# Kernel tuning notes

Measured on AMD Instinct MI355X. Metric: run time of the kernel, lower is better.

Reference implementation:

```python
import jax, jax.numpy as jnp
import numpy as np

B, C, H, W = 16, 1024, 48, 48
MID = 512
EPS = 1e-5


def _conv1x1(x, Wt, b):
    # x: [B,C,H,W], Wt: [O,C], b: [O] -> [B,O,H,W]
    return jnp.einsum('bchw,oc->bohw', x, Wt) + b[None, :, None, None]


def _bn_relu(y, gamma, beta, mean, var):
    inv = gamma / jnp.sqrt(var + EPS)
    return jax.nn.relu(y * inv[None, :, None, None] + (beta - mean * inv)[None, :, None, None])


def setup_inputs() -> dict:
    key = jax.random.key(0)
    ks = jax.random.split(key, 17)
    d = {
        'x': jax.random.normal(ks[0], (B, C, H, W), jnp.float32),
        'Wf': jax.random.normal(ks[1], (MID, C), jnp.float32) * (2.0 / C) ** 0.5,
        'bf': jax.random.normal(ks[2], (MID,), jnp.float32) * 0.1,
        'gf': jax.random.uniform(ks[3], (MID,), jnp.float32, 0.5, 1.5),
        'betaf': jax.random.normal(ks[4], (MID,), jnp.float32) * 0.1,
        'mf': jax.random.normal(ks[5], (MID,), jnp.float32) * 0.1,
        'vf': jax.random.uniform(ks[6], (MID,), jnp.float32, 0.5, 1.5),
        'Wg': jax.random.normal(ks[7], (MID, C), jnp.float32) * (2.0 / C) ** 0.5,
        'bg': jax.random.normal(ks[8], (MID,), jnp.float32) * 0.1,
        'gg': jax.random.uniform(ks[9], (MID,), jnp.float32, 0.5, 1.5),
        'betag': jax.random.normal(ks[10], (MID,), jnp.float32) * 0.1,
        'mg': jax.random.normal(ks[11], (MID,), jnp.float32) * 0.1,
        'vg': jax.random.uniform(ks[12], (MID,), jnp.float32, 0.5, 1.5),
        'Wh': jax.random.normal(ks[13], (MID, C), jnp.float32) * (2.0 / C) ** 0.5,
        'bh': jax.random.normal(ks[14], (MID,), jnp.float32) * 0.1,
        'Wv': jax.random.normal(ks[15], (C, MID), jnp.float32) * (2.0 / MID) ** 0.5,
        'bv': jax.random.normal(ks[16], (C,), jnp.float32) * 0.1,
    }
    return d


def reference(x, Wf, bf, gf, betaf, mf, vf, Wg, bg, gg, betag, mg, vg, Wh, bh, Wv, bv):
    b, c, h, w = x.shape
    n = h * w
    mid = Wf.shape[0]
    f_x = _bn_relu(_conv1x1(x, Wf, bf), gf, betaf, mf, vf).reshape(b, mid, n)  # [B,mid,N]
    g_x = _bn_relu(_conv1x1(x, Wg, bg), gg, betag, mg, vg).reshape(b, mid, n)  # [B,mid,N]
    h_x = _conv1x1(x, Wh, bh).reshape(b, mid, n)                               # [B,mid,N]
    # z = f_x^T @ g_x : [B,N,N]
    z = jnp.einsum('bmi,bmj->bij', f_x, g_x)
    attn = jax.nn.softmax(z * (mid ** -0.5), axis=-1)
    # attn @ h_x^T : [B,N,mid]
    out = jnp.einsum('bij,bmj->bim', attn, h_x)
    out = out.transpose(0, 2, 1).reshape(b, mid, h, w)
    out = _conv1x1(out, Wv, bv) + x  # residual
    return out
```

## Files before the change

### kernel.cpp

```cpp
#include <hip/hip_runtime.h>
#include <hip/hip_bf16.h>

#define BN_  16
#define CH   1024
#define MIDC 512
#define NPIX 2304

typedef __bf16 bf16x8 __attribute__((ext_vector_type(8)));
typedef __bf16 bf16x4 __attribute__((ext_vector_type(4)));
typedef float  f32x4  __attribute__((ext_vector_type(4)));

typedef __attribute__((address_space(1))) void void_g;
typedef __attribute__((address_space(3))) void void_l;

__device__ __forceinline__ void gll16(const void* g, void* l) {
  __builtin_amdgcn_global_load_lds((const void_g*)g, (void_l*)l, 16, 0, 0);
}

template<int EPI>
__global__ __launch_bounds__(256)
void gemm_bt(const __hip_bfloat16* __restrict__ Ag, int lda, long sA,
             const __hip_bfloat16* __restrict__ Bg, int ldb, long sB,
             void* __restrict__ Cg, int ldc, long sC,
             int K,
             const float* __restrict__ e0, const float* __restrict__ e1,
             const float* __restrict__ resid, long sR, float fscale)
{
  __shared__ __align__(16) __hip_bfloat16 lA[128 * 64];
  __shared__ __align__(16) __hip_bfloat16 lB[128 * 64];
  const int tid  = threadIdx.x;
  const int lane = tid & 63;
  const int wave = tid >> 6;

  const int gx = gridDim.x, gy = gridDim.y;
  const int nwg = gx * gy * gridDim.z;
  const int L  = blockIdx.x + gx * (blockIdx.y + gy * blockIdx.z);
  const int wg = (L & 7) * (nwg >> 3) + (L >> 3);
  const int pb = gx * gy;
  const int bz = wg / pb;
  const int rem = wg - bz * pb;
  const int m0 = (rem % gx) * 128;
  const int n0 = (rem / gx) * 128;

  const int srow = tid >> 3;
  const int schk = (tid & 7) ^ (srow & 7);
  const __hip_bfloat16* Ab = Ag + (long)bz * sA + (long)(m0 + srow) * lda + schk * 8;
  const __hip_bfloat16* Bb = Bg + (long)bz * sB + (long)(n0 + srow) * ldb + schk * 8;
  __hip_bfloat16* lAw = lA + wave * 512;
  __hip_bfloat16* lBw = lB + wave * 512;

  const int wr = wave >> 1, wc = wave & 1;
  const int fr = lane & 15;
  const int fc = lane >> 4;

  f32x4 acc[4][4] = {};

  for (int k0 = 0; k0 < K; k0 += 64) {
#pragma unroll
    for (int c = 0; c < 4; ++c) {
      gll16(Ab + k0 + (long)c * 32 * lda, lAw + c * 2048);
      gll16(Bb + k0 + (long)c * 32 * ldb, lBw + c * 2048);
    }
    __syncthreads();
#pragma unroll
    for (int kk = 0; kk < 2; ++kk) {
      bf16x8 af[4], bfv[4];
#pragma unroll
      for (int i = 0; i < 4; ++i) {
        const int ra = wr * 64 + i * 16 + fr;
        af[i]  = *(const bf16x8*)(lA + ra * 64 + (((kk * 4 + fc) ^ (fr & 7)) * 8));
        const int rb = wc * 64 + i * 16 + fr;
        bfv[i] = *(const bf16x8*)(lB + rb * 64 + (((kk * 4 + fc) ^ (fr & 7)) * 8));
      }
#pragma unroll
      for (int mi = 0; mi < 4; ++mi)
#pragma unroll
        for (int ni = 0; ni < 4; ++ni)
          acc[mi][ni] = __builtin_amdgcn_mfma_f32_16x16x32_bf16(af[mi], bfv[ni], acc[mi][ni], 0, 0, 0);
    }
    __syncthreads();
  }

  const int rbase = m0 + wr * 64 + (lane >> 4) * 4;
  const int cbase = n0 + wc * 64 + fr;
  if constexpr (EPI == 4) {
    float* Cb = (float*)Cg + (long)bz * sC;
    const float* Rb = resid + (long)bz * sR;
#pragma unroll
    for (int mi = 0; mi < 4; ++mi) {
#pragma unroll
      for (int r = 0; r < 4; ++r) {
        const int row = rbase + mi * 16 + r;
        const float bias = e0[row];
#pragma unroll
        for (int ni = 0; ni < 4; ++ni) {
          const long idx = (long)row * ldc + cbase + ni * 16;
          Cb[idx] = acc[mi][ni][r] + bias + Rb[idx];
        }
      }
    }
  } else {
    __hip_bfloat16* Cb = (__hip_bfloat16*)Cg + (long)bz * sC;
#pragma unroll
    for (int mi = 0; mi < 4; ++mi) {
#pragma unroll
      for (int r = 0; r < 4; ++r) {
        const int row = rbase + mi * 16 + r;
#pragma unroll
        for (int ni = 0; ni < 4; ++ni) {
          const int col = cbase + ni * 16;
          float v = acc[mi][ni][r];
          if constexpr (EPI == 1) { v = fmaxf(v * e0[col] + e1[col], 0.f); }
          if constexpr (EPI == 2) { v += e0[row]; }
          if constexpr (EPI == 3) { v *= fscale; }
          Cb[(long)row * ldc + col] = __float2bfloat16(v);
        }
      }
    }
  }
}

__global__ __launch_bounds__(256)
void softmax_rows(__hip_bfloat16* __restrict__ z)
{
  const long row = blockIdx.x;
  __hip_bfloat16* p = z + row * NPIX;
  const int t = threadIdx.x;
  const int lane = t & 63, wave = t >> 6;

  float v[9];
  bf16x8 pk = *(const bf16x8*)(p + t * 8);
#pragma unroll
  for (int i = 0; i < 8; ++i) v[i] = (float)pk[i];
  v[8] = __bfloat162float(p[2048 + t]);

  float mx = v[0];
#pragma unroll
  for (int i = 1; i < 9; ++i) mx = fmaxf(mx, v[i]);
#pragma unroll
  for (int o = 32; o > 0; o >>= 1) mx = fmaxf(mx, __shfl_xor(mx, o));
  __shared__ float redm[4], reds[4];
  if (lane == 0) redm[wave] = mx;
  __syncthreads();
  mx = fmaxf(fmaxf(redm[0], redm[1]), fmaxf(redm[2], redm[3]));

  float s = 0.f;
#pragma unroll
  for (int i = 0; i < 9; ++i) { v[i] = __expf(v[i] - mx); s += v[i]; }
#pragma unroll
  for (int o = 32; o > 0; o >>= 1) s += __shfl_xor(s, o);
  if (lane == 0) reds[wave] = s;
  __syncthreads();
  s = reds[0] + reds[1] + reds[2] + reds[3];
  const float inv = 1.f / s;

  bf16x8 ok;
#pragma unroll
  for (int i = 0; i < 8; ++i) ok[i] = (__bf16)(v[i] * inv);
  *(bf16x8*)(p + t * 8) = ok;
  p[2048 + t] = __float2bfloat16(v[8] * inv);
}

__global__ __launch_bounds__(256)
void transpose_cvt(const float* __restrict__ x, __hip_bfloat16* __restrict__ xt)
{
  __shared__ float tile[64 * 65];
  const int n0 = blockIdx.x * 64, c0 = blockIdx.y * 64;
  const long bo = (long)blockIdx.z * CH * NPIX;
  const int t = threadIdx.x;
#pragma unroll
  for (int i = 0; i < 16; ++i) {
    const int idx = i * 256 + t;
    const int cl = idx >> 6, nl = idx & 63;
    tile[cl * 65 + nl] = x[bo + (long)(c0 + cl) * NPIX + n0 + nl];
  }
  __syncthreads();
#pragma unroll
  for (int i = 0; i < 16; ++i) {
    const int idx = i * 256 + t;
    const int nl = idx >> 6, cl = idx & 63;
    xt[bo + (long)(n0 + nl) * CH + c0 + cl] = __float2bfloat16(tile[cl * 65 + nl]);
  }
}

__global__ __launch_bounds__(256)
void cvt4(const float* __restrict__ a, const float* __restrict__ b,
          const float* __restrict__ c, const float* __restrict__ d,
          __hip_bfloat16* oa, __hip_bfloat16* ob,
          __hip_bfloat16* oc, __hip_bfloat16* od)
{
  const int i = (blockIdx.x * 256 + threadIdx.x) * 4;
  const float* s; __hip_bfloat16* o;
  switch (blockIdx.y) {
    case 0:  s = a; o = oa; break;
    case 1:  s = b; o = ob; break;
    case 2:  s = c; o = oc; break;
    default: s = d; o = od; break;
  }
  const float4 v = *(const float4*)(s + i);
  bf16x4 w;
  w[0] = (__bf16)v.x; w[1] = (__bf16)v.y; w[2] = (__bf16)v.z; w[3] = (__bf16)v.w;
  *(bf16x4*)(o + i) = w;
}

__global__ void prep_scales(const float* bf_, const float* gf, const float* bef,
                            const float* mf, const float* vf,
                            const float* bg_, const float* gg, const float* beg,
                            const float* mg, const float* vg,
                            float* sc, float* sh)
{
  const int r = blockIdx.x * 256 + threadIdx.x;
  if (r >= 1024) return;
  int j; const float *b, *g, *be, *m, *vv;
  if (r < 512) { b = bf_; g = gf; be = bef; m = mf; vv = vf; j = r; }
  else         { b = bg_; g = gg; be = beg; m = mg; vv = vg; j = r - 512; }
  const float inv = g[j] / sqrtf(vv[j] + 1e-5f);
  sc[r] = inv;
  sh[r] = (b[j] - m[j]) * inv + be[j];
}

extern "C" void kernel_launch(void* const* d_in, const int* in_sizes, int n_in,
                              void* d_out, int out_size, void* d_ws, size_t ws_size,
                              hipStream_t stream)
{
  const float* x     = (const float*)d_in[0];
  const float* Wf    = (const float*)d_in[1];
  const float* bf_   = (const float*)d_in[2];
  const float* gf    = (const float*)d_in[3];
  const float* betaf = (const float*)d_in[4];
  const float* mf    = (const float*)d_in[5];
  const float* vf    = (const float*)d_in[6];
  const float* Wg    = (const float*)d_in[7];
  const float* bg_   = (const float*)d_in[8];
  const float* gg    = (const float*)d_in[9];
  const float* betag = (const float*)d_in[10];
  const float* mg    = (const float*)d_in[11];
  const float* vg    = (const float*)d_in[12];
  const float* Wh    = (const float*)d_in[13];
  const float* bh    = (const float*)d_in[14];
  const float* Wv    = (const float*)d_in[15];
  const float* bv    = (const float*)d_in[16];
  float* out = (float*)d_out;
  (void)in_sizes; (void)n_in; (void)out_size; (void)ws_size;

  char* ws = (char*)d_ws;
  size_t off = 0;
  auto take = [&](size_t bytes) -> char* {
    char* p = ws + off;
    off += (bytes + 255) & ~(size_t)255;
    return p;
  };
  __hip_bfloat16* xt   = (__hip_bfloat16*)take((size_t)BN_ * NPIX * CH * 2);
  __hip_bfloat16* fgT  = (__hip_bfloat16*)take((size_t)BN_ * NPIX * 1024 * 2);
  __hip_bfloat16* hbuf = (__hip_bfloat16*)take((size_t)BN_ * MIDC * NPIX * 2);
  __hip_bfloat16* om   = (__hip_bfloat16*)take((size_t)BN_ * NPIX * MIDC * 2);
  __hip_bfloat16* zat  = (__hip_bfloat16*)take((size_t)BN_ * NPIX * NPIX * 2);
  __hip_bfloat16* Wfgb = (__hip_bfloat16*)take((size_t)1024 * CH * 2);
  __hip_bfloat16* Whb  = (__hip_bfloat16*)take((size_t)MIDC * CH * 2);
  __hip_bfloat16* Wvb  = (__hip_bfloat16*)take((size_t)CH * MIDC * 2);
  float* scfg = (float*)take(1024 * 4);
  float* shfg = (float*)take(1024 * 4);

  prep_scales<<<dim3(4), dim3(256), 0, stream>>>(bf_, gf, betaf, mf, vf,
                                                 bg_, gg, betag, mg, vg, scfg, shfg);
  cvt4<<<dim3(512, 4), dim3(256), 0, stream>>>(Wf, Wg, Wh, Wv,
                                               Wfgb, Wfgb + 512 * 1024, Whb, Wvb);
  transpose_cvt<<<dim3(36, 16, BN_), dim3(256), 0, stream>>>(x, xt);

  gemm_bt<1><<<dim3(18, 8, BN_), dim3(256), 0, stream>>>(
      xt, CH, (long)NPIX * CH, Wfgb, CH, 0L,
      fgT, 1024, (long)NPIX * 1024, CH,
      scfg, shfg, nullptr, 0L, 0.f);

  gemm_bt<2><<<dim3(4, 18, BN_), dim3(256), 0, stream>>>(
      Whb, CH, 0L, xt, CH, (long)NPIX * CH,
      hbuf, NPIX, (long)MIDC * NPIX, CH,
      bh, nullptr, nullptr, 0L, 0.f);

  gemm_bt<3><<<dim3(18, 18, BN_), dim3(256), 0, stream>>>(
      fgT, 1024, (long)NPIX * 1024, fgT + 512, 1024, (long)NPIX * 1024,
      zat, NPIX, (long)NPIX * NPIX, MIDC,
      nullptr, nullptr, nullptr, 0L, 0.044194173824159216f);

  softmax_rows<<<dim3(BN_ * NPIX), dim3(256), 0, stream>>>(zat);

  gemm_bt<0><<<dim3(18, 4, BN_), dim3(256), 0, stream>>>(
      zat, NPIX, (long)NPIX * NPIX, hbuf, NPIX, (long)MIDC * NPIX,
      om, MIDC, (long)NPIX * MIDC, NPIX,
      nullptr, nullptr, nullptr, 0L, 0.f);

  gemm_bt<4><<<dim3(8, 18, BN_), dim3(256), 0, stream>>>(
      Wvb, MIDC, 0L, om, MIDC, (long)NPIX * MIDC,
      out, NPIX, (long)CH * NPIX, MIDC,
      bv, nullptr, x, (long)CH * NPIX, 0.f);
}
```

Before: 604.9 us.

## Replace 128x128 GEMM with double-buffered 256x256 tile, 8-wave kernel

The GEMM moves from 128x128 tiles with 4 waves and single-buffered LDS to 256x256 tiles with 8 waves and a double-buffered 128KB LDS. Global-to-LDS loads for the next K-step are interleaved with the MFMA phases, and s_setprio raises priority during the MFMA bursts. The aim is more data reuse per tile and overlap of memory loads with compute, replacing the full syncthreads stalls. In exchange, each workgroup holds more accumulator registers and LDS, so occupancy drops to one block per CU, and the small GEMMs launch fewer workgroups.

```diff
diff --git a/kernel.cpp b/kernel.cpp
--- a/kernel.cpp
+++ b/kernel.cpp
@@ -18,19 +18,18 @@
 }
 
 template<int EPI>
-__global__ __launch_bounds__(256)
-void gemm_bt(const __hip_bfloat16* __restrict__ Ag, int lda, long sA,
+__global__ __launch_bounds__(512)
+void gemm256(const __hip_bfloat16* __restrict__ Ag, int lda, long sA,
              const __hip_bfloat16* __restrict__ Bg, int ldb, long sB,
              void* __restrict__ Cg, int ldc, long sC,
              int K,
              const float* __restrict__ e0, const float* __restrict__ e1,
              const float* __restrict__ resid, long sR, float fscale)
 {
-  __shared__ __align__(16) __hip_bfloat16 lA[128 * 64];
-  __shared__ __align__(16) __hip_bfloat16 lB[128 * 64];
-  const int tid  = threadIdx.x;
-  const int lane = tid & 63;
-  const int wave = tid >> 6;
+  __shared__ __align__(16) __hip_bfloat16 lds[65536];
+  const int tid = threadIdx.x;
+  const int l   = tid & 63;
+  const int w   = tid >> 6;
 
   const int gx = gridDim.x, gy = gridDim.y;
   const int nwg = gx * gy * gridDim.z;
@@ -39,62 +38,95 @@
   const int pb = gx * gy;
   const int bz = wg / pb;
   const int rem = wg - bz * pb;
-  const int m0 = (rem % gx) * 128;
-  const int n0 = (rem / gx) * 128;
-
-  const int srow = tid >> 3;
-  const int schk = (tid & 7) ^ (srow & 7);
+  const int m0 = (rem % gx) * 256;
+  const int n0 = (rem / gx) * 256;
+
+  const int srow = w * 8 + (l >> 3);
+  const int schk = (l & 7) ^ (l >> 3);
   const __hip_bfloat16* Ab = Ag + (long)bz * sA + (long)(m0 + srow) * lda + schk * 8;
   const __hip_bfloat16* Bb = Bg + (long)bz * sB + (long)(n0 + srow) * ldb + schk * 8;
-  __hip_bfloat16* lAw = lA + wave * 512;
-  __hip_bfloat16* lBw = lB + wave * 512;
-
-  const int wr = wave >> 1, wc = wave & 1;
-  const int fr = lane & 15;
-  const int fc = lane >> 4;
-
-  f32x4 acc[4][4] = {};
-
-  for (int k0 = 0; k0 < K; k0 += 64) {
-#pragma unroll
-    for (int c = 0; c < 4; ++c) {
-      gll16(Ab + k0 + (long)c * 32 * lda, lAw + c * 2048);
-      gll16(Bb + k0 + (long)c * 32 * ldb, lBw + c * 2048);
+  const int stg = w * 512;
+
+  auto stageA = [&](int buf, int half, long kofs) {
+    __hip_bfloat16* d = lds + buf * 16384 + half * 8192 + stg;
+    gll16(Ab + kofs + (long)(half * 128) * lda,      d);
+    gll16(Ab + kofs + (long)(half * 128 + 64) * lda, d + 4096);
+  };
+  auto stageB = [&](int buf, int half, long kofs) {
+    __hip_bfloat16* d = lds + 32768 + buf * 16384 + half * 8192 + stg;
+    gll16(Bb + kofs + (long)(half * 128) * ldb,      d);
+    gll16(Bb + kofs + (long)(half * 128 + 64) * ldb, d + 4096);
+  };
+
+  const int wr = w >> 2, wc = w & 3;
+  const int fr = l & 15;
+  const int fc = l >> 4;
+  const int slot0 = ((fc)     ^ (fr & 7)) * 8;
+  const int slot1 = ((4 + fc) ^ (fr & 7)) * 8;
+
+  f32x4 acc[8][4] = {};
+
+  stageA(0, 0, 0); stageA(0, 1, 0); stageB(0, 0, 0); stageB(0, 1, 0);
+  asm volatile("s_waitcnt vmcnt(0)" ::: "memory");
+  __builtin_amdgcn_s_barrier();
+
+  const int NT = K >> 6;
+  for (int t = 0; t < NT; ++t) {
+    const __hip_bfloat16* lAc = lds + (t & 1) * 16384;
+    const __hip_bfloat16* lBc = lds + 32768 + (t & 1) * 16384;
+    const int  nb   = (t & 1) ^ 1;
+    const long knxt = (long)(t + 1) * 64;
+    const bool more = (t + 1 < NT);
+#pragma unroll
+    for (int p = 0; p < 4; ++p) {
+      const int mh = p >> 1, nh = p & 1;
+      bf16x8 avA[4][2], avB[2][2];
+#pragma unroll
+      for (int i = 0; i < 4; ++i) {
+        const int row = wr * 128 + (mh * 4 + i) * 16 + fr;
+        avA[i][0] = *(const bf16x8*)(lAc + row * 64 + slot0);
+        avA[i][1] = *(const bf16x8*)(lAc + row * 64 + slot1);
+      }
+#pragma unroll
+      for (int j = 0; j < 2; ++j) {
+        const int row = wc * 64 + (nh * 2 + j) * 16 + fr;
+        avB[j][0] = *(const bf16x8*)(lBc + row * 64 + slot0);
+        avB[j][1] = *(const bf16x8*)(lBc + row * 64 + slot1);
+      }
+      if (more) {
+        if (p < 2) stageA(nb, p, knxt); else stageB(nb, p - 2, knxt);
+      }
+      __builtin_amdgcn_s_barrier();
+      __builtin_amdgcn_s_setprio(1);
+#pragma unroll
+      for (int i = 0; i < 4; ++i)
+#pragma unroll
+        for (int j = 0; j < 2; ++j) {
+          acc[mh * 4 + i][nh * 2 + j] = __builtin_amdgcn_mfma_f32_16x16x32_bf16(
+              avA[i][0], avB[j][0], acc[mh * 4 + i][nh * 2 + j], 0, 0, 0);
+          acc[mh * 4 + i][nh * 2 + j] = __builtin_amdgcn_mfma_f32_16x16x32_bf16(
+              avA[i][1], avB[j][1], acc[mh * 4 + i][nh * 2 + j], 0, 0, 0);
+        }
+      __builtin_amdgcn_s_setprio(0);
+      if (p == 3) asm volatile("s_waitcnt vmcnt(0)" ::: "memory");
+      __builtin_amdgcn_s_barrier();
     }
-    __syncthreads();
-#pragma unroll
-    for (int kk = 0; kk < 2; ++kk) {
-      bf16x8 af[4], bfv[4];
-#pragma unroll
-      for (int i = 0; i < 4; ++i) {
-        const int ra = wr * 64 + i * 16 + fr;
-        af[i]  = *(const bf16x8*)(lA + ra * 64 + (((kk * 4 + fc) ^ (fr & 7)) * 8));
-        const int rb = wc * 64 + i * 16 + fr;
-        bfv[i] = *(const bf16x8*)(lB + rb * 64 + (((kk * 4 + fc) ^ (fr & 7)) * 8));
-      }
-#pragma unroll
-      for (int mi = 0; mi < 4; ++mi)
-#pragma unroll
-        for (int ni = 0; ni < 4; ++ni)
-          acc[mi][ni] = __builtin_amdgcn_mfma_f32_16x16x32_bf16(af[mi], bfv[ni], acc[mi][ni], 0, 0, 0);
-    }
-    __syncthreads();
-  }
-
-  const int rbase = m0 + wr * 64 + (lane >> 4) * 4;
-  const int cbase = n0 + wc * 64 + fr;
+  }
+
+  const int rb0 = m0 + wr * 128 + (l >> 4) * 4;
+  const int cb0 = n0 + wc * 64 + fr;
   if constexpr (EPI == 4) {
     float* Cb = (float*)Cg + (long)bz * sC;
     const float* Rb = resid + (long)bz * sR;
 #pragma unroll
-    for (int mi = 0; mi < 4; ++mi) {
+    for (int mi = 0; mi < 8; ++mi) {
 #pragma unroll
       for (int r = 0; r < 4; ++r) {
-        const int row = rbase + mi * 16 + r;
+        const int row = rb0 + mi * 16 + r;
         const float bias = e0[row];
 #pragma unroll
         for (int ni = 0; ni < 4; ++ni) {
-          const long idx = (long)row * ldc + cbase + ni * 16;
+          const long idx = (long)row * ldc + cb0 + ni * 16;
           Cb[idx] = acc[mi][ni][r] + bias + Rb[idx];
         }
       }
@@ -102,13 +134,13 @@
   } else {
     __hip_bfloat16* Cb = (__hip_bfloat16*)Cg + (long)bz * sC;
 #pragma unroll
-    for (int mi = 0; mi < 4; ++mi) {
+    for (int mi = 0; mi < 8; ++mi) {
 #pragma unroll
       for (int r = 0; r < 4; ++r) {
-        const int row = rbase + mi * 16 + r;
+        const int row = rb0 + mi * 16 + r;
 #pragma unroll
         for (int ni = 0; ni < 4; ++ni) {
-          const int col = cbase + ni * 16;
+          const int col = cb0 + ni * 16;
           float v = acc[mi][ni][r];
           if constexpr (EPI == 1) { v = fmaxf(v * e0[col] + e1[col], 0.f); }
           if constexpr (EPI == 2) { v += e0[row]; }
@@ -198,9 +230,9 @@
     default: s = d; o = od; break;
   }
   const float4 v = *(const float4*)(s + i);
-  bf16x4 w;
-  w[0] = (__bf16)v.x; w[1] = (__bf16)v.y; w[2] = (__bf16)v.z; w[3] = (__bf16)v.w;
-  *(bf16x4*)(o + i) = w;
+  bf16x4 wv;
+  wv[0] = (__bf16)v.x; wv[1] = (__bf16)v.y; wv[2] = (__bf16)v.z; wv[3] = (__bf16)v.w;
+  *(bf16x4*)(o + i) = wv;
 }
 
 __global__ void prep_scales(const float* bf_, const float* gf, const float* bef,
@@ -267,29 +299,29 @@
                                                Wfgb, Wfgb + 512 * 1024, Whb, Wvb);
   transpose_cvt<<<dim3(36, 16, BN_), dim3(256), 0, stream>>>(x, xt);
 
-  gemm_bt<1><<<dim3(18, 8, BN_), dim3(256), 0, stream>>>(
+  gemm256<1><<<dim3(9, 4, BN_), dim3(512), 0, stream>>>(
       xt, CH, (long)NPIX * CH, Wfgb, CH, 0L,
       fgT, 1024, (long)NPIX * 1024, CH,
       scfg, shfg, nullptr, 0L, 0.f);
 
-  gemm_bt<2><<<dim3(4, 18, BN_), dim3(256), 0, stream>>>(
+  gemm256<2><<<dim3(2, 9, BN_), dim3(512), 0, stream>>>(
       Whb, CH, 0L, xt, CH, (long)NPIX * CH,
       hbuf, NPIX, (long)MIDC * NPIX, CH,
       bh, nullptr, nullptr, 0L, 0.f);
 
-  gemm_bt<3><<<dim3(18, 18, BN_), dim3(256), 0, stream>>>(
+  gemm256<3><<<dim3(9, 9, BN_), dim3(512), 0, stream>>>(
       fgT, 1024, (long)NPIX * 1024, fgT + 512, 1024, (long)NPIX * 1024,
       zat, NPIX, (long)NPIX * NPIX, MIDC,
       nullptr, nullptr, nullptr, 0L, 0.044194173824159216f);
 
   softmax_rows<<<dim3(BN_ * NPIX), dim3(256), 0, stream>>>(zat);
 
-  gemm_bt<0><<<dim3(18, 4, BN_), dim3(256), 0, stream>>>(
+  gemm256<0><<<dim3(9, 2, BN_), dim3(512), 0, stream>>>(
       zat, NPIX, (long)NPIX * NPIX, hbuf, NPIX, (long)MIDC * NPIX,
       om, MIDC, (long)NPIX * MIDC, NPIX,
       nullptr, nullptr, nullptr, 0L, 0.f);
 
-  gemm_bt<4><<<dim3(8, 18, BN_), dim3(256), 0, stream>>>(
+  gemm256<4><<<dim3(4, 9, BN_), dim3(512), 0, stream>>>(
       Wvb, MIDC, 0L, om, MIDC, (long)NPIX * MIDC,
       out, NPIX, (long)CH * NPIX, MIDC,
       bv, nullptr, x, (long)CH * NPIX, 0.f);
```

After: 681.7 us. +12.7%, slower.

## Fuse softmax exponent into QK GEMM epilogue and defer normalization to PV GEMM

Applied to the files above, without the earlier changes.

The attention score GEMM epilogue now computes exp2 of the scaled logits directly, stores the unnormalized values, and writes per-tile partial row sums. A small kernel reduces the partials to inverse row sums, which the PV GEMM epilogue applies to each output row. This removes the standalone softmax pass that read and rewrote the full NxN score matrix. It drops the max-subtraction, so it relies on the logits being small enough not to overflow in exp.

```diff
diff --git a/kernel.cpp b/kernel.cpp
--- a/kernel.cpp
+++ b/kernel.cpp
@@ -5,6 +5,7 @@
 #define CH   1024
 #define MIDC 512
 #define NPIX 2304
+#define NCHK 36
 
 typedef __bf16 bf16x8 __attribute__((ext_vector_type(8)));
 typedef __bf16 bf16x4 __attribute__((ext_vector_type(4)));
@@ -24,7 +25,8 @@
              void* __restrict__ Cg, int ldc, long sC,
              int K,
              const float* __restrict__ e0, const float* __restrict__ e1,
-             const float* __restrict__ resid, long sR, float fscale)
+             const float* __restrict__ resid, long sR, float fscale,
+             float* __restrict__ pw)
 {
   __shared__ __align__(16) __hip_bfloat16 lA[128 * 64];
   __shared__ __align__(16) __hip_bfloat16 lB[128 * 64];
@@ -99,6 +101,27 @@
         }
       }
     }
+  } else if constexpr (EPI == 6) {
+    __hip_bfloat16* Cb = (__hip_bfloat16*)Cg + (long)bz * sC;
+    float* pp = pw + ((long)bz * NCHK + (n0 >> 6) + wc) * NPIX;
+#pragma unroll
+    for (int mi = 0; mi < 4; ++mi) {
+#pragma unroll
+      for (int r = 0; r < 4; ++r) {
+        const int row = rbase + mi * 16 + r;
+        float rs = 0.f;
+#pragma unroll
+        for (int ni = 0; ni < 4; ++ni) {
+          const int col = cbase + ni * 16;
+          const float ev = exp2f(acc[mi][ni][r] * fscale);
+          rs += ev;
+          Cb[(long)row * ldc + col] = __float2bfloat16(ev);
+        }
+#pragma unroll
+        for (int o = 1; o < 16; o <<= 1) rs += __shfl_xor(rs, o);
+        if (fr == 0) pp[row] = rs;
+      }
+    }
   } else {
     __hip_bfloat16* Cb = (__hip_bfloat16*)Cg + (long)bz * sC;
 #pragma unroll
@@ -106,13 +129,15 @@
 #pragma unroll
       for (int r = 0; r < 4; ++r) {
         const int row = rbase + mi * 16 + r;
+        float rsc = 0.f;
+        if constexpr (EPI == 5) { rsc = e0[(long)bz * NPIX + row]; }
 #pragma unroll
         for (int ni = 0; ni < 4; ++ni) {
           const int col = cbase + ni * 16;
           float v = acc[mi][ni][r];
           if constexpr (EPI == 1) { v = fmaxf(v * e0[col] + e1[col], 0.f); }
           if constexpr (EPI == 2) { v += e0[row]; }
-          if constexpr (EPI == 3) { v *= fscale; }
+          if constexpr (EPI == 5) { v *= rsc; }
           Cb[(long)row * ldc + col] = __float2bfloat16(v);
         }
       }
@@ -121,44 +146,15 @@
 }
 
 __global__ __launch_bounds__(256)
-void softmax_rows(__hip_bfloat16* __restrict__ z)
-{
-  const long row = blockIdx.x;
-  __hip_bfloat16* p = z + row * NPIX;
-  const int t = threadIdx.x;
-  const int lane = t & 63, wave = t >> 6;
-
-  float v[9];
-  bf16x8 pk = *(const bf16x8*)(p + t * 8);
-#pragma unroll
-  for (int i = 0; i < 8; ++i) v[i] = (float)pk[i];
-  v[8] = __bfloat162float(p[2048 + t]);
-
-  float mx = v[0];
-#pragma unroll
-  for (int i = 1; i < 9; ++i) mx = fmaxf(mx, v[i]);
-#pragma unroll
-  for (int o = 32; o > 0; o >>= 1) mx = fmaxf(mx, __shfl_xor(mx, o));
-  __shared__ float redm[4], reds[4];
-  if (lane == 0) redm[wave] = mx;
-  __syncthreads();
-  mx = fmaxf(fmaxf(redm[0], redm[1]), fmaxf(redm[2], redm[3]));
-
+void reduce_invs(const float* __restrict__ pp, float* __restrict__ invS)
+{
+  const int row = blockIdx.x * 256 + threadIdx.x;
+  const int b   = blockIdx.y;
+  const float* p = pp + (long)b * NCHK * NPIX;
   float s = 0.f;
 #pragma unroll
-  for (int i = 0; i < 9; ++i) { v[i] = __expf(v[i] - mx); s += v[i]; }
-#pragma unroll
-  for (int o = 32; o > 0; o >>= 1) s += __shfl_xor(s, o);
-  if (lane == 0) reds[wave] = s;
-  __syncthreads();
-  s = reds[0] + reds[1] + reds[2] + reds[3];
-  const float inv = 1.f / s;
-
-  bf16x8 ok;
-#pragma unroll
-  for (int i = 0; i < 8; ++i) ok[i] = (__bf16)(v[i] * inv);
-  *(bf16x8*)(p + t * 8) = ok;
-  p[2048 + t] = __float2bfloat16(v[8] * inv);
+  for (int c = 0; c < NCHK; ++c) s += p[(long)c * NPIX + row];
+  invS[(long)b * NPIX + row] = 1.f / s;
 }
 
 __global__ __launch_bounds__(256)
@@ -198,9 +194,9 @@
     default: s = d; o = od; break;
   }
   const float4 v = *(const float4*)(s + i);
-  bf16x4 w;
-  w[0] = (__bf16)v.x; w[1] = (__bf16)v.y; w[2] = (__bf16)v.z; w[3] = (__bf16)v.w;
-  *(bf16x4*)(o + i) = w;
+  bf16x4 wv;
+  wv[0] = (__bf16)v.x; wv[1] = (__bf16)v.y; wv[2] = (__bf16)v.z; wv[3] = (__bf16)v.w;
+  *(bf16x4*)(o + i) = wv;
 }
 
 __global__ void prep_scales(const float* bf_, const float* gf, const float* bef,
@@ -260,6 +256,8 @@
   __hip_bfloat16* Wvb  = (__hip_bfloat16*)take((size_t)CH * MIDC * 2);
   float* scfg = (float*)take(1024 * 4);
   float* shfg = (float*)take(1024 * 4);
+  float* partials = (float*)take((size_t)BN_ * NCHK * NPIX * 4);
+  float* invS     = (float*)take((size_t)BN_ * NPIX * 4);
 
   prep_scales<<<dim3(4), dim3(256), 0, stream>>>(bf_, gf, betaf, mf, vf,
                                                  bg_, gg, betag, mg, vg, scfg, shfg);
@@ -270,27 +268,28 @@
   gemm_bt<1><<<dim3(18, 8, BN_), dim3(256), 0, stream>>>(
       xt, CH, (long)NPIX * CH, Wfgb, CH, 0L,
       fgT, 1024, (long)NPIX * 1024, CH,
-      scfg, shfg, nullptr, 0L, 0.f);
+      scfg, shfg, nullptr, 0L, 0.f, nullptr);
 
   gemm_bt<2><<<dim3(4, 18, BN_), dim3(256), 0, stream>>>(
       Whb, CH, 0L, xt, CH, (long)NPIX * CH,
       hbuf, NPIX, (long)MIDC * NPIX, CH,
-      bh, nullptr, nullptr, 0L, 0.f);
-
-  gemm_bt<3><<<dim3(18, 18, BN_), dim3(256), 0, stream>>>(
+      bh, nullptr, nullptr, 0L, 0.f, nullptr);
+
+  const float sc_log2e = (float)(0.044194173824159216 * 1.4426950408889634);
+  gemm_bt<6><<<dim3(18, 18, BN_), dim3(256), 0, stream>>>(
       fgT, 1024, (long)NPIX * 1024, fgT + 512, 1024, (long)NPIX * 1024,
       zat, NPIX, (long)NPIX * NPIX, MIDC,
-      nullptr, nullptr, nullptr, 0L, 0.044194173824159216f);
-
-  softmax_rows<<<dim3(BN_ * NPIX), dim3(256), 0, stream>>>(zat);
-
-  gemm_bt<0><<<dim3(18, 4, BN_), dim3(256), 0, stream>>>(
+      nullptr, nullptr, nullptr, 0L, sc_log2e, partials);
+
+  reduce_invs<<<dim3(NPIX / 256, BN_), dim3(256), 0, stream>>>(partials, invS);
+
+  gemm_bt<5><<<dim3(18, 4, BN_), dim3(256), 0, stream>>>(
       zat, NPIX, (long)NPIX * NPIX, hbuf, NPIX, (long)MIDC * NPIX,
       om, MIDC, (long)NPIX * MIDC, NPIX,
-      nullptr, nullptr, nullptr, 0L, 0.f);
+      invS, nullptr, nullptr, 0L, 0.f, nullptr);
 
   gemm_bt<4><<<dim3(8, 18, BN_), dim3(256), 0, stream>>>(
       Wvb, MIDC, 0L, om, MIDC, (long)NPIX * MIDC,
       out, NPIX, (long)CH * NPIX, MIDC,
-      bv, nullptr, x, (long)CH * NPIX, 0.f);
-}
+      bv, nullptr, x, (long)CH * NPIX, 0.f, nullptr);
+}
```

Result: no change. 606.8 us (+0.3%).
